# Kernel tuning notes

Hardware: AMD Instinct MI355X
Metric: run time of the kernel (lower is better)

Reference implementation:

```python
import jax, jax.numpy as jnp
import numpy as np

B, S, D, H = 64, 256, 2048, 16
HD = D // H

def setup_inputs() -> dict:
    key = jax.random.key(0)
    k1, k2, k3 = jax.random.split(key, 3)
    x = jax.random.normal(k1, (B, S, D), dtype=jnp.float32)
    # torch Linear weights: [out_features, in_features], scaled like kaiming-ish init
    w_qkv = jax.random.normal(k2, (3 * D, D), dtype=jnp.float32) * (1.0 / np.sqrt(D))
    w_o = jax.random.normal(k3, (D, D), dtype=jnp.float32) * (1.0 / np.sqrt(D))
    return {"x": x, "w_qkv": w_qkv, "w_o": w_o}

def reference(x, w_qkv, w_o):
    b, s, d = x.shape
    qkv = jnp.einsum('bsd,ed->bse', x, w_qkv)            # [B,S,3D]
    qkv = qkv.reshape(b, s, 3, H, HD).transpose(2, 0, 3, 1, 4)  # [3,B,H,S,HD]
    q, k, v = qkv[0], qkv[1], qkv[2]
    scores = jnp.einsum('bhqd,bhkd->bhqk', q, k) * (HD ** -0.5)  # [B,H,S,S]
    causal = jnp.triu(jnp.ones((s, s), dtype=bool), 1)
    scores = jnp.where(causal, jnp.float32(-1e9), scores)
    a = jax.nn.softmax(scores, axis=-1)
    ctx = jnp.einsum('bhqk,bhkd->bhqd', a, v)            # [B,H,S,HD]
    ctx = ctx.transpose(0, 2, 1, 3).reshape(b, s, d)     # [B,S,D]
    return jnp.einsum('bsd,ed->bse', ctx, w_o)
```

## Files before the change

kernel.cpp:

```cpp
#include <hip/hip_runtime.h>

#define NB 64
#define NS 256
#define ND 2048
#define NH 16
#define NHD 128

typedef unsigned short ushort_t;
typedef __attribute__((ext_vector_type(8))) __bf16 bf16x8;
typedef __attribute__((ext_vector_type(4))) short shortx4;
typedef __attribute__((ext_vector_type(4))) float f32x4;
typedef __attribute__((ext_vector_type(4))) unsigned short ushortx4;

__device__ __forceinline__ unsigned short f2bf(float f) {
  union { float f; unsigned int u; } v; v.f = f;
  unsigned int r = v.u + 0x7FFFu + ((v.u >> 16) & 1u);
  return (unsigned short)(r >> 16);
}

__device__ __forceinline__ void gload16(const void* g, void* l) {
  __builtin_amdgcn_global_load_lds(
      (__attribute__((address_space(1))) void*)(void*)(g),
      (__attribute__((address_space(3))) void*)(l), 16, 0, 0);
}

__global__ void cast_f32_bf16(const float* __restrict__ in, ushort_t* __restrict__ out, long n) {
  long i = ((long)blockIdx.x * blockDim.x + threadIdx.x) * 4;
  if (i + 3 < n) {
    float4 v = *reinterpret_cast<const float4*>(in + i);
    ushortx4 o;
    o.x = f2bf(v.x); o.y = f2bf(v.y); o.z = f2bf(v.z); o.w = f2bf(v.w);
    *reinterpret_cast<ushortx4*>(out + i) = o;
  }
}

template<int MODE>
__global__ __launch_bounds__(512, 2) void gemm256(const ushort_t* __restrict__ A,
                                                  const ushort_t* __restrict__ Bt,
                                                  float* __restrict__ Cf,
                                                  ushort_t* __restrict__ Cq,
                                                  int M, int N, int K) {
  extern __shared__ char smem[];
  const int tid = threadIdx.x;
  const int wv = tid >> 6, lane = tid & 63;
  const int l15 = lane & 15, lg = lane >> 4;
  const int wm = wv >> 2, wn = wv & 3;

  const int nbn = N >> 8;
  const int nwg = (M >> 8) * nbn;
  const int bid = blockIdx.x;
  const int q8 = nwg >> 3, r8 = nwg & 7;
  const int xcd = bid & 7, lin = bid >> 3;
  const int wg = (xcd < r8 ? xcd * (q8 + 1) : r8 * (q8 + 1) + (xcd - r8) * q8) + lin;
  const int m0 = (wg / nbn) << 8;
  const int n0 = (wg % nbn) << 8;

  const int srow = wv * 16 + (lane >> 2);
  const int sce = ((lane & 3) * 8) ^ (((srow >> 1) & 3) << 3);
  const ushort_t* pa0 = A  + (long)(m0 + srow) * K + sce;
  const ushort_t* pa1 = pa0 + (long)128 * K;
  const ushort_t* pb0 = Bt + (long)(n0 + srow) * K + sce;
  const ushort_t* pb1 = pb0 + (long)128 * K;

  const int c = (lg * 16) ^ (((l15 >> 1) & 3) << 4);

  f32x4 acc[8][4] = {};
  const int nkt = K >> 5;

  {
    char* d0 = smem + wv * 1024;
    gload16(pa0, d0);
    gload16(pa1, d0 + 8192);
    gload16(pb0, d0 + 16384);
    gload16(pb1, d0 + 16384 + 8192);
    char* d1 = smem + 32768 + wv * 1024;
    gload16(pa0 + 32, d1);
    gload16(pa1 + 32, d1 + 8192);
    gload16(pb0 + 32, d1 + 16384);
    gload16(pb1 + 32, d1 + 16384 + 8192);
  }
  asm volatile("s_waitcnt vmcnt(4)" ::: "memory");
  __builtin_amdgcn_s_barrier();

  int buf = 0;
  for (int t = 0; t < nkt; ++t) {
    const int so = buf * 32768;
    const bool pf = (t + 2 < nkt);
    const int pb = (buf + 2 >= 3) ? buf - 1 : buf + 2;
    bf16x8 af[4], bfr[4];
    #pragma unroll
    for (int i = 0; i < 4; ++i)
      af[i] = *reinterpret_cast<const bf16x8*>(smem + so + (wm * 128 + i * 16 + l15) * 64 + c);
    #pragma unroll
    for (int j = 0; j < 4; ++j)
      bfr[j] = *reinterpret_cast<const bf16x8*>(smem + so + 16384 + (wn * 64 + j * 16 + l15) * 64 + c);
    if (pf) {
      char* d = smem + pb * 32768 + wv * 1024;
      gload16(pa0 + (t + 2) * 32, d);
      gload16(pa1 + (t + 2) * 32, d + 8192);
    }
    __builtin_amdgcn_s_barrier();
    asm volatile("s_waitcnt lgkmcnt(0)" ::: "memory");
    __builtin_amdgcn_sched_barrier(0);
    __builtin_amdgcn_s_setprio(1);
    #pragma unroll
    for (int i = 0; i < 4; ++i)
      #pragma unroll
      for (int j = 0; j < 4; ++j)
        acc[i][j] = __builtin_amdgcn_mfma_f32_16x16x32_bf16(af[i], bfr[j], acc[i][j], 0, 0, 0);
    __builtin_amdgcn_s_setprio(0);
    __builtin_amdgcn_s_barrier();
    bf16x8 ag[4];
    #pragma unroll
    for (int i = 0; i < 4; ++i)
      ag[i] = *reinterpret_cast<const bf16x8*>(smem + so + (wm * 128 + 64 + i * 16 + l15) * 64 + c);
    if (pf) {
      char* d = smem + pb * 32768 + 16384 + wv * 1024;
      gload16(pb0 + (t + 2) * 32, d);
      gload16(pb1 + (t + 2) * 32, d + 8192);
    }
    __builtin_amdgcn_s_barrier();
    asm volatile("s_waitcnt lgkmcnt(0)" ::: "memory");
    __builtin_amdgcn_sched_barrier(0);
    __builtin_amdgcn_s_setprio(1);
    #pragma unroll
    for (int i = 0; i < 4; ++i)
      #pragma unroll
      for (int j = 0; j < 4; ++j)
        acc[4 + i][j] = __builtin_amdgcn_mfma_f32_16x16x32_bf16(ag[i], bfr[j], acc[4 + i][j], 0, 0, 0);
    __builtin_amdgcn_s_setprio(0);
    if (pf) asm volatile("s_waitcnt vmcnt(4)" ::: "memory");
    else    asm volatile("s_waitcnt vmcnt(0)" ::: "memory");
    __builtin_amdgcn_s_barrier();
    buf = (buf + 1 == 3) ? 0 : buf + 1;
  }

  #pragma unroll
  for (int k = 0; k < 8; ++k) {
    const int mrow = m0 + wm * 128 + (k >> 2) * 64 + (k & 3) * 16 + lg * 4;
    #pragma unroll
    for (int j = 0; j < 4; ++j) {
      const int n = n0 + wn * 64 + j * 16 + l15;
      #pragma unroll
      for (int r = 0; r < 4; ++r) {
        const int m = mrow + r;
        const float v = acc[k][j][r];
        if (MODE == 0) {
          Cf[(long)m * N + n] = v;
        } else {
          const int tq = n >> 11, hh = (n >> 7) & 15, hd = n & 127;
          const int b = m >> 8, s = m & 255;
          Cq[((((long)tq * NB + b) * NH + hh) * NS + s) * NHD + hd] = f2bf(v);
        }
      }
    }
  }
}

__global__ __launch_bounds__(512) void attn_fused(const ushort_t* __restrict__ qkv,
                                                  ushort_t* __restrict__ ctx) {
  const int bh = blockIdx.x;
  const int b = bh >> 4, h = bh & 15;
  const int wave = threadIdx.x >> 6, lane = threadIdx.x & 63;
  const int l15 = lane & 15, lg = lane >> 4;
  const long head_off = ((long)(b * NH + h)) * (NS * NHD);
  const ushort_t* Qp = qkv + head_off;
  const ushort_t* Kp = qkv + (long)NB * NH * NS * NHD + head_off;
  const ushort_t* Vp = qkv + 2L * NB * NH * NS * NHD + head_off;
  const int q0 = wave * 32;

  bf16x8 qf[2][4];
  #pragma unroll
  for (int ni = 0; ni < 2; ++ni)
    #pragma unroll
    for (int kk = 0; kk < 4; ++kk)
      qf[ni][kk] = *reinterpret_cast<const bf16x8*>(Qp + (q0 + ni * 16 + l15) * NHD + kk * 32 + lg * 8);

  f32x4 o[8][2] = {};
  float mstate[2] = {-1e30f, -1e30f};
  float lstate[2] = {0.f, 0.f};
  const float scale = 0.08838834764831845f;
  const int ntiles = (q0 + 32 + 63) >> 6;

  for (int kt = 0; kt < ntiles; ++kt) {
    f32x4 st[4][2] = {};
    #pragma unroll
    for (int kk = 0; kk < 4; ++kk) {
      bf16x8 kf[4];
      #pragma unroll
      for (int mi = 0; mi < 4; ++mi)
        kf[mi] = *reinterpret_cast<const bf16x8*>(Kp + (kt * 64 + mi * 16 + l15) * NHD + kk * 32 + lg * 8);
      #pragma unroll
      for (int mi = 0; mi < 4; ++mi)
        #pragma unroll
        for (int ni = 0; ni < 2; ++ni)
          st[mi][ni] = __builtin_amdgcn_mfma_f32_16x16x32_bf16(kf[mi], qf[ni][kk], st[mi][ni], 0, 0, 0);
    }
    const bool last = (kt == ntiles - 1);
    #pragma unroll
    for (int mi = 0; mi < 4; ++mi)
      #pragma unroll
      for (int ni = 0; ni < 2; ++ni)
        #pragma unroll
        for (int r = 0; r < 4; ++r) {
          const int kc = kt * 64 + mi * 16 + lg * 4 + r;
          const int q = q0 + ni * 16 + l15;
          float v = st[mi][ni][r] * scale;
          if (last && kc > q) v = -1e30f;
          st[mi][ni][r] = v;
        }
    shortx4 p[4][2];
    #pragma unroll
    for (int ni = 0; ni < 2; ++ni) {
      float tmax = -1e30f;
      #pragma unroll
      for (int mi = 0; mi < 4; ++mi)
        #pragma unroll
        for (int r = 0; r < 4; ++r) tmax = fmaxf(tmax, st[mi][ni][r]);
      tmax = fmaxf(tmax, __shfl_xor(tmax, 16, 64));
      tmax = fmaxf(tmax, __shfl_xor(tmax, 32, 64));
      const float mnew = fmaxf(mstate[ni], tmax);
      const float alpha = __expf(mstate[ni] - mnew);
      float tsum = 0.f;
      #pragma unroll
      for (int mi = 0; mi < 4; ++mi)
        #pragma unroll
        for (int r = 0; r < 4; ++r) {
          const float pe = __expf(st[mi][ni][r] - mnew);
          st[mi][ni][r] = pe;
          tsum += pe;
        }
      tsum += __shfl_xor(tsum, 16, 64);
      tsum += __shfl_xor(tsum, 32, 64);
      lstate[ni] = lstate[ni] * alpha + tsum;
      mstate[ni] = mnew;
      #pragma unroll
      for (int f = 0; f < 8; ++f)
        #pragma unroll
        for (int r = 0; r < 4; ++r) o[f][ni][r] *= alpha;
      #pragma unroll
      for (int mi = 0; mi < 4; ++mi)
        #pragma unroll
        for (int r = 0; r < 4; ++r) p[mi][ni][r] = (short)f2bf(st[mi][ni][r]);
    }
    #pragma unroll
    for (int f = 0; f < 8; ++f)
      #pragma unroll
      for (int mi = 0; mi < 4; ++mi) {
        shortx4 vt;
        #pragma unroll
        for (int j = 0; j < 4; ++j)
          vt[j] = (short)Vp[(kt * 64 + mi * 16 + lg * 4 + j) * NHD + f * 16 + l15];
        #pragma unroll
        for (int ni = 0; ni < 2; ++ni)
          o[f][ni] = __builtin_amdgcn_mfma_f32_16x16x16bf16_1k(vt, p[mi][ni], o[f][ni], 0, 0, 0);
      }
  }
  const float inv0 = 1.f / lstate[0], inv1 = 1.f / lstate[1];
  #pragma unroll
  for (int f = 0; f < 8; ++f)
    #pragma unroll
    for (int ni = 0; ni < 2; ++ni) {
      const float inv = ni ? inv1 : inv0;
      const int q = q0 + ni * 16 + l15;
      const int hd = f * 16 + lg * 4;
      ushortx4 ov;
      #pragma unroll
      for (int r = 0; r < 4; ++r) ov[r] = f2bf(o[f][ni][r] * inv);
      *reinterpret_cast<ushortx4*>(ctx + ((long)(b * NS + q)) * ND + h * NHD + hd) = ov;
    }
}

extern "C" void kernel_launch(void* const* d_in, const int* in_sizes, int n_in,
                              void* d_out, int out_size, void* d_ws, size_t ws_size,
                              hipStream_t stream) {
  const float* x     = (const float*)d_in[0];
  const float* w_qkv = (const float*)d_in[1];
  const float* w_o   = (const float*)d_in[2];
  char* ws = (char*)d_ws;
  if (ws_size < 369098752UL) return;
  ushort_t* xb    = (ushort_t*)(ws);
  ushort_t* wqkvb = (ushort_t*)(ws + 67108864L);
  ushort_t* wob   = (ushort_t*)(ws + 92274688L);
  ushort_t* qkvb  = (ushort_t*)(ws + 100663296L);
  ushort_t* ctxb  = (ushort_t*)(ws + 301989888L);

  const long nx = (long)NB * NS * ND;
  const long nq = 3L * ND * ND;
  const long no = (long)ND * ND;
  cast_f32_bf16<<<dim3(nx / 1024), 256, 0, stream>>>(x, xb, nx);
  cast_f32_bf16<<<dim3(nq / 1024), 256, 0, stream>>>(w_qkv, wqkvb, nq);
  cast_f32_bf16<<<dim3(no / 1024), 256, 0, stream>>>(w_o, wob, no);

  const int lds_bytes = 3 * 32768;
  (void)hipFuncSetAttribute(reinterpret_cast<const void*>(&gemm256<1>),
                            hipFuncAttributeMaxDynamicSharedMemorySize, lds_bytes);
  (void)hipFuncSetAttribute(reinterpret_cast<const void*>(&gemm256<0>),
                            hipFuncAttributeMaxDynamicSharedMemorySize, lds_bytes);

  gemm256<1><<<dim3(64 * 24), 512, lds_bytes, stream>>>(xb, wqkvb, nullptr, qkvb,
                                                        NB * NS, 3 * ND, ND);
  attn_fused<<<dim3(NB * NH), 512, 0, stream>>>(qkvb, ctxb);
  gemm256<0><<<dim3(64 * 8), 512, lds_bytes, stream>>>(ctxb, wob, (float*)d_out, nullptr,
                                                       NB * NS, ND, ND);
}
```

Before: 707.0 us.

## Restructure GEMM mainloop with 4-stage LDS ring and register double-buffered fragments

Replaces the 3-buffer GEMM mainloop, which used two barrier-separated half-steps per k-tile, with a 4-buffer LDS ring that prefetches three tiles ahead. Fragments for the next tile are loaded from LDS into a second register set while the current tile's 32 MFMAs issue, so there is one barrier per k-tile instead of several. The aim is to hide LDS read latency and cut synchronization overhead. In exchange it raises LDS to 128KB and roughly doubles the fragment registers, which can reduce occupancy or cause spills.

```diff
diff --git a/kernel.cpp b/kernel.cpp
--- a/kernel.cpp
+++ b/kernel.cpp
@@ -67,77 +67,75 @@
   f32x4 acc[8][4] = {};
   const int nkt = K >> 5;
 
-  {
-    char* d0 = smem + wv * 1024;
-    gload16(pa0, d0);
-    gload16(pa1, d0 + 8192);
-    gload16(pb0, d0 + 16384);
-    gload16(pb1, d0 + 16384 + 8192);
-    char* d1 = smem + 32768 + wv * 1024;
-    gload16(pa0 + 32, d1);
-    gload16(pa1 + 32, d1 + 8192);
-    gload16(pb0 + 32, d1 + 16384);
-    gload16(pb1 + 32, d1 + 16384 + 8192);
-  }
+  bf16x8 faA[8], faB[4], fbA[8], fbB[4];
+
+  #pragma unroll
+  for (int tt = 0; tt < 3; ++tt) {
+    char* d = smem + tt * 32768 + wv * 1024;
+    const long ko = (long)tt * 32;
+    gload16(pa0 + ko, d);
+    gload16(pa1 + ko, d + 8192);
+    gload16(pb0 + ko, d + 16384);
+    gload16(pb1 + ko, d + 24576);
+  }
+  asm volatile("s_waitcnt vmcnt(8)" ::: "memory");
+  __builtin_amdgcn_s_barrier();
+  __builtin_amdgcn_sched_barrier(0);
+  #pragma unroll
+  for (int i = 0; i < 8; ++i)
+    faA[i] = *reinterpret_cast<const bf16x8*>(smem + (wm * 128 + i * 16 + l15) * 64 + c);
+  #pragma unroll
+  for (int j = 0; j < 4; ++j)
+    faB[j] = *reinterpret_cast<const bf16x8*>(smem + 16384 + (wn * 64 + j * 16 + l15) * 64 + c);
   asm volatile("s_waitcnt vmcnt(4)" ::: "memory");
-  __builtin_amdgcn_s_barrier();
-
-  int buf = 0;
-  for (int t = 0; t < nkt; ++t) {
-    const int so = buf * 32768;
-    const bool pf = (t + 2 < nkt);
-    const int pb = (buf + 2 >= 3) ? buf - 1 : buf + 2;
-    bf16x8 af[4], bfr[4];
-    #pragma unroll
-    for (int i = 0; i < 4; ++i)
-      af[i] = *reinterpret_cast<const bf16x8*>(smem + so + (wm * 128 + i * 16 + l15) * 64 + c);
-    #pragma unroll
-    for (int j = 0; j < 4; ++j)
-      bfr[j] = *reinterpret_cast<const bf16x8*>(smem + so + 16384 + (wn * 64 + j * 16 + l15) * 64 + c);
-    if (pf) {
-      char* d = smem + pb * 32768 + wv * 1024;
-      gload16(pa0 + (t + 2) * 32, d);
-      gload16(pa1 + (t + 2) * 32, d + 8192);
-    }
-    __builtin_amdgcn_s_barrier();
-    asm volatile("s_waitcnt lgkmcnt(0)" ::: "memory");
-    __builtin_amdgcn_sched_barrier(0);
-    __builtin_amdgcn_s_setprio(1);
-    #pragma unroll
-    for (int i = 0; i < 4; ++i)
-      #pragma unroll
-      for (int j = 0; j < 4; ++j)
-        acc[i][j] = __builtin_amdgcn_mfma_f32_16x16x32_bf16(af[i], bfr[j], acc[i][j], 0, 0, 0);
-    __builtin_amdgcn_s_setprio(0);
-    __builtin_amdgcn_s_barrier();
-    bf16x8 ag[4];
-    #pragma unroll
-    for (int i = 0; i < 4; ++i)
-      ag[i] = *reinterpret_cast<const bf16x8*>(smem + so + (wm * 128 + 64 + i * 16 + l15) * 64 + c);
-    if (pf) {
-      char* d = smem + pb * 32768 + 16384 + wv * 1024;
-      gload16(pb0 + (t + 2) * 32, d);
-      gload16(pb1 + (t + 2) * 32, d + 8192);
-    }
-    __builtin_amdgcn_s_barrier();
-    asm volatile("s_waitcnt lgkmcnt(0)" ::: "memory");
-    __builtin_amdgcn_sched_barrier(0);
-    __builtin_amdgcn_s_setprio(1);
-    #pragma unroll
-    for (int i = 0; i < 4; ++i)
-      #pragma unroll
-      for (int j = 0; j < 4; ++j)
-        acc[4 + i][j] = __builtin_amdgcn_mfma_f32_16x16x32_bf16(ag[i], bfr[j], acc[4 + i][j], 0, 0, 0);
-    __builtin_amdgcn_s_setprio(0);
-    if (pf) asm volatile("s_waitcnt vmcnt(4)" ::: "memory");
-    else    asm volatile("s_waitcnt vmcnt(0)" ::: "memory");
-    __builtin_amdgcn_s_barrier();
-    buf = (buf + 1 == 3) ? 0 : buf + 1;
-  }
+
+#define TILE(T_, CA_, CB_, NA_, NB_)                                           \
+  {                                                                            \
+    const int t_ = (T_);                                                       \
+    __builtin_amdgcn_s_barrier();                                              \
+    __builtin_amdgcn_sched_barrier(0);                                         \
+    if (t_ + 3 < nkt) {                                                        \
+      char* d = smem + ((t_ + 3) & 3) * 32768 + wv * 1024;                     \
+      const long ko = (long)(t_ + 3) * 32;                                     \
+      gload16(pa0 + ko, d);                                                    \
+      gload16(pa1 + ko, d + 8192);                                             \
+      gload16(pb0 + ko, d + 16384);                                            \
+      gload16(pb1 + ko, d + 24576);                                            \
+    }                                                                          \
+    if (t_ + 1 < nkt) {                                                        \
+      const char* rb = smem + ((t_ + 1) & 3) * 32768;                          \
+      _Pragma("unroll")                                                        \
+      for (int i = 0; i < 8; ++i)                                              \
+        NA_[i] = *reinterpret_cast<const bf16x8*>(rb + (wm * 128 + i * 16 + l15) * 64 + c); \
+      _Pragma("unroll")                                                        \
+      for (int j = 0; j < 4; ++j)                                              \
+        NB_[j] = *reinterpret_cast<const bf16x8*>(rb + 16384 + (wn * 64 + j * 16 + l15) * 64 + c); \
+      asm volatile("s_waitcnt lgkmcnt(12)" ::: "memory");                      \
+    } else {                                                                   \
+      asm volatile("s_waitcnt lgkmcnt(0)" ::: "memory");                       \
+    }                                                                          \
+    __builtin_amdgcn_sched_barrier(0);                                         \
+    __builtin_amdgcn_s_setprio(1);                                             \
+    _Pragma("unroll")                                                          \
+    for (int i = 0; i < 8; ++i)                                                \
+      _Pragma("unroll")                                                        \
+      for (int j = 0; j < 4; ++j)                                              \
+        acc[i][j] = __builtin_amdgcn_mfma_f32_16x16x32_bf16(CA_[i], CB_[j], acc[i][j], 0, 0, 0); \
+    __builtin_amdgcn_s_setprio(0);                                             \
+    __builtin_amdgcn_sched_barrier(0);                                         \
+    if (t_ + 3 < nkt) asm volatile("s_waitcnt vmcnt(4)" ::: "memory");         \
+    else              asm volatile("s_waitcnt vmcnt(0)" ::: "memory");         \
+  }
+
+  for (int t = 0; t < nkt; t += 2) {
+    TILE(t,     faA, faB, fbA, fbB);
+    TILE(t + 1, fbA, fbB, faA, faB);
+  }
+#undef TILE
 
   #pragma unroll
   for (int k = 0; k < 8; ++k) {
-    const int mrow = m0 + wm * 128 + (k >> 2) * 64 + (k & 3) * 16 + lg * 4;
+    const int mrow = m0 + wm * 128 + k * 16 + lg * 4;
     #pragma unroll
     for (int j = 0; j < 4; ++j) {
       const int n = n0 + wn * 64 + j * 16 + l15;
@@ -292,7 +290,7 @@
   cast_f32_bf16<<<dim3(nq / 1024), 256, 0, stream>>>(w_qkv, wqkvb, nq);
   cast_f32_bf16<<<dim3(no / 1024), 256, 0, stream>>>(w_o, wob, no);
 
-  const int lds_bytes = 3 * 32768;
+  const int lds_bytes = 4 * 32768;
   (void)hipFuncSetAttribute(reinterpret_cast<const void*>(&gemm256<1>),
                             hipFuncAttributeMaxDynamicSharedMemorySize, lds_bytes);
   (void)hipFuncSetAttribute(reinterpret_cast<const void*>(&gemm256<0>),
```

Result: no change. 705.9 us (-0.2%).
